# Optimization experiments

Measured on AMD Instinct MI355X. Metric: run time of the kernel, lower is better.

Reference implementation:

```python
import jax, jax.numpy as jnp
import numpy as np

IMAGE_W = 256
IMAGE_H = 256
SIGMA = 0.2
EPS = 1e-07


def _gauss_filter(g, size, psize, pad):
    """g: [B,N] center coords in pixels. Returns [B,N,size,psize]."""
    # grid coords over padded canvas: value i - pad at row i (matches np.indices - pad)
    coords = jnp.arange(size + 2 * pad, dtype=jnp.float32) - pad          # [size+2pad]
    offs = jnp.arange(1, psize + 1, dtype=jnp.float32) - psize / 2 - 0.5  # [psize]
    mu = g[:, :, None] + offs[None, None, :]                              # [B,N,psize]
    F = jnp.exp(-(coords[None, None, :, None] - mu[:, :, None, :]) ** 2 / (2 * SIGMA ** 2))
    F = F / (F.sum(axis=2, keepdims=True) + EPS)
    return F[:, :, pad:size + pad]                                        # [B,N,size,psize]


def setup_inputs() -> dict:
    key = jax.random.key(0)
    k1, k2 = jax.random.split(key)
    brushes = jax.random.uniform(k1, (32, 64, 2), dtype=jnp.float32)
    patches = jax.random.normal(k2, (32, 64, 3, 16, 16), dtype=jnp.float32)
    return {"brushes": brushes, "patches": patches}


def reference(brushes, patches):
    B, N, C, ph, pw = patches.shape
    pad = ph // 2  # pad='half_patch'
    gx = brushes[:, :, 0] * IMAGE_W  # [B,N]
    gy = brushes[:, :, 1] * IMAGE_H
    Fx = _gauss_filter(gx, IMAGE_W, pw, pad)  # [B,N,w,pw]
    Fy = _gauss_filter(gy, IMAGE_H, ph, pad)  # [B,N,h,ph]
    # contract over pw: [B,N,C,w,ph]
    t = jnp.einsum('bnwq,bncpq->bncwp', Fx, patches)
    # contract over ph: [B,N,C,w,h]
    out = jnp.einsum('bncwp,bnhp->bncwh', t, Fy)
    out = out.mean(axis=1)            # [B,C,w,h]
    out = jnp.swapaxes(out, 2, 3)     # [B,C,h,w]
    return out
```

## Files before the change

### kernel.cpp

```cpp
#include <hip/hip_runtime.h>
#include <hip/hip_bf16.h>


#define TILE 16

__global__ __launch_bounds__(256) void brush_tile(
        const float* __restrict__ brushes,
        const float* __restrict__ patches,
        float* __restrict__ out)
{
    const int b   = blockIdx.z;
    const int tx  = blockIdx.x * TILE;
    const int ty  = blockIdx.y * TILE;
    const int tid = threadIdx.x;
    const int w   = tx + (tid & 15);
    const int h   = ty + (tid >> 4);

    __shared__ float gxy[128];
    __shared__ unsigned long long smask;
    __shared__ float sp[768];
    __shared__ float invZ[32];

    if (tid < 128) gxy[tid] = brushes[(b << 7) + tid] * 256.0f;
    __syncthreads();

    if (tid < 64) {
        const float gx = gxy[2 * tid], gy = gxy[2 * tid + 1];
        const bool hit =
            (gx >= (float)tx - 9.5f) & (gx <= (float)tx + 24.5f) &
            (gy >= (float)ty - 9.5f) & (gy <= (float)ty + 24.5f);
        const unsigned long long m = __ballot(hit);
        if (tid == 0) smask = m;
    }
    __syncthreads();
    unsigned long long mask = smask;

    float acc0 = 0.0f, acc1 = 0.0f, acc2 = 0.0f;
    const float fw = (float)w, fh = (float)h;

    while (mask) {
        const int n = __builtin_ctzll(mask);
        mask &= mask - 1;
        const float gx = gxy[2 * n], gy = gxy[2 * n + 1];

        const float* pb = patches + (size_t)((b << 6) + n) * 768;
        if (tid < 192) {
            ((float4*)sp)[tid] = ((const float4*)pb)[tid];
        } else if (tid < 224) {
            const int t = tid - 192;
            const int axis = t >> 4, q = t & 15;
            const float g  = axis ? gy : gx;
            const float mu = g + (float)q - 7.5f;
            const float fl = floorf(mu);
            float Z = 0.0f;
#pragma unroll
            for (int d = -1; d <= 2; ++d) {
                const float c = fl + (float)d;
                if (c >= -8.0f && c <= 263.0f) {
                    const float u = c - mu;
                    Z += __expf(-12.5f * u * u);
                }
            }
            invZ[t] = 1.0f / (Z + 1e-7f);
        }
        __syncthreads();

        const float ax = fw - gx + 7.5f;
        const float ay = fh - gy + 7.5f;
        if (ax >= -2.0f && ax <= 17.0f && ay >= -2.0f && ay <= 17.0f) {
            const int qlo = max(0, (int)ceilf(ax - 2.0f));
            const int qhi = min(15, (int)floorf(ax + 2.0f));
            const int plo = max(0, (int)ceilf(ay - 2.0f));
            const int phi = min(15, (int)floorf(ay + 2.0f));
            const int nq = qhi - qlo + 1;
            float wx[5];
            for (int j = 0; j < nq; ++j) {
                const float d = ax - (float)(qlo + j);
                wx[j] = __expf(-12.5f * d * d) * invZ[qlo + j];
            }
            for (int p = plo; p <= phi; ++p) {
                const float d  = ay - (float)p;
                const float wy = __expf(-12.5f * d * d) * invZ[16 + p];
                const float* row = &sp[(p << 4) + qlo];
                float s0 = 0.0f, s1 = 0.0f, s2 = 0.0f;
                for (int j = 0; j < nq; ++j) {
                    const float t = wx[j];
                    s0 += t * row[j];
                    s1 += t * row[256 + j];
                    s2 += t * row[512 + j];
                }
                acc0 += wy * s0;
                acc1 += wy * s1;
                acc2 += wy * s2;
            }
        }
        __syncthreads();
    }

    const float sc = 1.0f / 64.0f;
    float* ob = out + (((size_t)(b * 3)) << 16) + (h << 8) + w;
    ob[0]       = acc0 * sc;
    ob[1 << 16] = acc1 * sc;
    ob[2 << 16] = acc2 * sc;
}

extern "C" void kernel_launch(void* const* d_in, const int* in_sizes, int n_in,
                              void* d_out, int out_size, void* d_ws, size_t ws_size,
                              hipStream_t stream) {
    const float* brushes = (const float*)d_in[0];
    const float* patches = (const float*)d_in[1];
    float* out = (float*)d_out;
    brush_tile<<<dim3(16, 16, 32), dim3(256), 0, stream>>>(brushes, patches, out);
}
```

Measured before the change: 89.35 us.

## Split brush splat into separable two-pass contraction with recurrence-based Gaussian weights

Replaces the per-pixel 2D windowed loop with two separable passes through shared memory. The first contracts the patch along x into a per-column intermediate, the second contracts along y. Gaussian weights are generated with a multiplicative recurrence instead of one exp per tap. Fixed 5-tap unrolled loops over zero-padded float4 rows remove the divergent variable-length loops. The cost is an extra shared-memory pass and barrier per brush, plus possible accuracy drift from the recurrence.

```diff
diff --git a/kernel.cpp b/kernel.cpp
--- a/kernel.cpp
+++ b/kernel.cpp
@@ -16,12 +16,17 @@
     const int w   = tx + (tid & 15);
     const int h   = ty + (tid >> 4);
 
-    __shared__ float gxy[128];
+    __shared__ float  gxy[128];
     __shared__ unsigned long long smask;
-    __shared__ float sp[768];
-    __shared__ float invZ[32];
+    __shared__ float4 sp4[16 * 21];
+    __shared__ float4 T4 [16 * 21];
+    __shared__ float  invZ[32];
 
-    if (tid < 128) gxy[tid] = brushes[(b << 7) + tid] * 256.0f;
+    if (tid < 32) {
+        float4 v = ((const float4*)(brushes + (b << 7)))[tid];
+        v.x *= 256.0f; v.y *= 256.0f; v.z *= 256.0f; v.w *= 256.0f;
+        ((float4*)gxy)[tid] = v;
+    }
     __syncthreads();
 
     if (tid < 64) {
@@ -36,7 +41,8 @@
     unsigned long long mask = smask;
 
     float acc0 = 0.0f, acc1 = 0.0f, acc2 = 0.0f;
-    const float fw = (float)w, fh = (float)h;
+    const float fh = (float)h;
+    const float E25 = 1.3887944e-11f;
 
     while (mask) {
         const int n = __builtin_ctzll(mask);
@@ -44,11 +50,12 @@
         const float gx = gxy[2 * n], gy = gxy[2 * n + 1];
 
         const float* pb = patches + (size_t)((b << 6) + n) * 768;
-        if (tid < 192) {
-            ((float4*)sp)[tid] = ((const float4*)pb)[tid];
-        } else if (tid < 224) {
-            const int t = tid - 192;
-            const int axis = t >> 4, q = t & 15;
+        const float r0 = pb[tid];
+        const float r1 = pb[tid + 256];
+        const float r2 = pb[tid + 512];
+
+        if (tid < 32) {
+            const int axis = tid >> 4, q = tid & 15;
             const float g  = axis ? gy : gx;
             const float mu = g + (float)q - 7.5f;
             const float fl = floorf(mu);
@@ -61,40 +68,62 @@
                     Z += __expf(-12.5f * u * u);
                 }
             }
-            invZ[t] = 1.0f / (Z + 1e-7f);
+            invZ[tid] = 1.0f / (Z + 1e-7f);
         }
         __syncthreads();
 
-        const float ax = fw - gx + 7.5f;
-        const float ay = fh - gy + 7.5f;
-        if (ax >= -2.0f && ax <= 17.0f && ay >= -2.0f && ay <= 17.0f) {
-            const int qlo = max(0, (int)ceilf(ax - 2.0f));
-            const int qhi = min(15, (int)floorf(ax + 2.0f));
-            const int plo = max(0, (int)ceilf(ay - 2.0f));
-            const int phi = min(15, (int)floorf(ay + 2.0f));
-            const int nq = qhi - qlo + 1;
-            float wx[5];
-            for (int j = 0; j < nq; ++j) {
-                const float d = ax - (float)(qlo + j);
-                wx[j] = __expf(-12.5f * d * d) * invZ[qlo + j];
+        {
+            const int q = tid & 15, p = tid >> 4;
+            const float zx = invZ[q];
+            sp4[p * 21 + q] = make_float4(r0 * zx, r1 * zx, r2 * zx, 0.0f);
+            if (tid < 64)
+                sp4[(tid >> 2) * 21 + 16 + (tid & 3)] = make_float4(0, 0, 0, 0);
+        }
+        __syncthreads();
+
+        {
+            const int wi = tid & 15, p = tid >> 4;
+            const float ax = (float)(tx + wi) - gx + 7.5f;
+            float4 s = make_float4(0, 0, 0, 0);
+            if (ax >= -2.5f && ax <= 17.5f) {
+                int qlo = (int)ceilf(ax - 2.0f);
+                qlo = qlo < 0 ? 0 : (qlo > 15 ? 15 : qlo);
+                const float d0 = ax - (float)qlo;
+                float wgt = __expf(-12.5f * d0 * d0);
+                float u   = __expf(25.0f * d0 - 12.5f);
+                const float4* row = &sp4[p * 21 + qlo];
+#pragma unroll
+                for (int j = 0; j < 5; ++j) {
+                    const float4 v = row[j];
+                    s.x += wgt * v.x; s.y += wgt * v.y; s.z += wgt * v.z;
+                    wgt *= u; u *= E25;
+                }
+                const float zy = invZ[16 + p];
+                s.x *= zy; s.y *= zy; s.z *= zy;
             }
-            for (int p = plo; p <= phi; ++p) {
-                const float d  = ay - (float)p;
-                const float wy = __expf(-12.5f * d * d) * invZ[16 + p];
-                const float* row = &sp[(p << 4) + qlo];
-                float s0 = 0.0f, s1 = 0.0f, s2 = 0.0f;
-                for (int j = 0; j < nq; ++j) {
-                    const float t = wx[j];
-                    s0 += t * row[j];
-                    s1 += t * row[256 + j];
-                    s2 += t * row[512 + j];
+            T4[wi * 21 + p] = s;
+            if (tid < 64)
+                T4[(tid >> 2) * 21 + 16 + (tid & 3)] = make_float4(0, 0, 0, 0);
+        }
+        __syncthreads();
+
+        {
+            const float ay = fh - gy + 7.5f;
+            if (ay >= -2.5f && ay <= 17.5f) {
+                int plo = (int)ceilf(ay - 2.0f);
+                plo = plo < 0 ? 0 : (plo > 15 ? 15 : plo);
+                const float d0 = ay - (float)plo;
+                float wgt = __expf(-12.5f * d0 * d0);
+                float u   = __expf(25.0f * d0 - 12.5f);
+                const float4* row = &T4[(tid & 15) * 21 + plo];
+#pragma unroll
+                for (int j = 0; j < 5; ++j) {
+                    const float4 v = row[j];
+                    acc0 += wgt * v.x; acc1 += wgt * v.y; acc2 += wgt * v.z;
+                    wgt *= u; u *= E25;
                 }
-                acc0 += wy * s0;
-                acc1 += wy * s1;
-                acc2 += wy * s2;
             }
         }
-        __syncthreads();
     }
 
     const float sc = 1.0f / 64.0f;
```

Result: faster. 79.40 us (-11.1%).
